# Optimization experiments

Measured on AMD Instinct MI355X. Metric: run time of the kernel, lower is better.

Reference implementation:

```python
import jax, jax.numpy as jnp
import numpy as np

# Config (matches init_kwargs): range [-32,32]^3, voxel 0.5 -> 128^3 grid; BEV 200x200
PC_LOW = np.array([-32.0, -32.0, -32.0], dtype=np.float32)
PC_HIGH = np.array([32.0, 32.0, 32.0], dtype=np.float32)
VOX = 0.5
G = 128
BEV_H, BEV_W = 200, 200
BN_EPS = 1e-5
STRIDES = [1, 2, 1, 2, 1, 1]


def setup_inputs() -> dict:
    key = jax.random.key(0)
    ks = jax.random.split(key, 10)
    N = 2_000_000
    xyz = jax.random.uniform(ks[0], (N, 3), jnp.float32, minval=-32.0, maxval=32.0)
    inten = jax.random.uniform(ks[1], (N, 1), jnp.float32)
    points = jnp.concatenate([xyz, inten], axis=1)  # (N,4)
    chans = [(32, 4), (64, 32), (64, 64), (128, 64), (128, 128), (256, 128)]
    inp = {"points": points}
    for i, (co, ci) in enumerate(chans):
        fan_in = ci * 27
        inp[f"w{i+1}"] = jax.random.normal(ks[2 + i], (co, ci, 3, 3, 3), jnp.float32) / np.sqrt(fan_in)
        inp[f"g{i+1}"] = jnp.ones((co,), jnp.float32)
        inp[f"b{i+1}"] = jnp.zeros((co,), jnp.float32)
    return inp


def _voxelize(points):
    # range filtering + floor-binning + clamp, faithful to voxelize_points (dense path: scatter-ADD)
    low = jnp.asarray(PC_LOW)
    high = jnp.asarray(PC_HIGH)
    mask = jnp.all((points[:, :3] >= low) & (points[:, :3] <= high), axis=1)
    coords = jnp.floor((points[:, :3] - low) / VOX).astype(jnp.int32)
    coords = jnp.clip(coords, 0, G - 1)
    vals = points * mask[:, None].astype(points.dtype)  # invalid points contribute 0
    # original indexes voxel_grid[:, z, y, x]
    grid = jnp.zeros((G, G, G, 4), points.dtype)
    grid = grid.at[coords[:, 2], coords[:, 1], coords[:, 0]].add(vals)
    return jnp.transpose(grid, (3, 0, 1, 2))  # (4, G, G, G)


def _conv3d(x, w, s):
    # PyTorch Conv3d(k=3, padding=1, stride=s), NCDHW
    return jax.lax.conv_general_dilated(
        x, w, window_strides=(s, s, s), padding=[(1, 1), (1, 1), (1, 1)],
        dimension_numbers=("NCDHW", "OIDHW", "NCDHW"))


def _bn_relu(x, g, b):
    # eval-mode BN: running_mean=0, running_var=1
    scale = (g / jnp.sqrt(1.0 + BN_EPS))[None, :, None, None, None]
    return jax.nn.relu(x * scale + b[None, :, None, None, None])


def reference(points, w1, w2, w3, w4, w5, w6,
              g1, g2, g3, g4, g5, g6,
              b1, b2, b3, b4, b5, b6):
    ws = [w1, w2, w3, w4, w5, w6]
    gs = [g1, g2, g3, g4, g5, g6]
    bs = [b1, b2, b3, b4, b5, b6]
    x = _voxelize(points)[None]  # (1,4,G,G,G)
    for w, g, b, s in zip(ws, gs, bs, STRIDES):
        x = _bn_relu(_conv3d(x, w, s), g, b)
    feat = x[0]  # (256, G/4, G/4, G/4)
    bev = jnp.max(feat, axis=2)  # torch.max(..., dim=2) on (C,D1,D2,D3) -> (C,D1,D3)
    # F.interpolate bilinear align_corners=False == jax.image.resize half-pixel bilinear
    bev = jax.image.resize(bev, (bev.shape[0], BEV_H, BEV_W), method="bilinear")
    return bev
```

## Files before the change

### kernel.cpp

```cpp
#include <hip/hip_runtime.h>
#include <hip/hip_fp16.h>
#include <cstdint>
#include <cstddef>

typedef __attribute__((ext_vector_type(8))) short short8;
typedef __attribute__((ext_vector_type(8))) _Float16 half8;
typedef __attribute__((ext_vector_type(16))) float f32x16;

__device__ __forceinline__ float bf2f(unsigned short u) { return __uint_as_float(((unsigned)u) << 16); }
__device__ __forceinline__ unsigned short f2bf(float f) {
    unsigned u = __float_as_uint(f);
    return (unsigned short)((u + 0x7fffu + ((u >> 16) & 1u)) >> 16);
}
__device__ __forceinline__ void sync_lds() {
    asm volatile("s_waitcnt lgkmcnt(0)\n\ts_barrier" ::: "memory");
}

static constexpr float BN_INV = 0.9999950000374997f;


__device__ __forceinline__ int vox_bucket(float4 p, bool& ok) {
    ok = !(p.x < -32.f || p.x > 32.f || p.y < -32.f || p.y > 32.f || p.z < -32.f || p.z > 32.f);
    int cy = min(max((int)floorf((p.y + 32.f) * 2.f), 0), 127);
    int cz = min(max((int)floorf((p.z + 32.f) * 2.f), 0), 127);
    return cz * 4 + (cy >> 5);
}

__global__ __launch_bounds__(256) void vox_count(const float4* __restrict__ pts,
                                                 int* __restrict__ cnt, int N) {
    __shared__ int h[512];
    for (int t = threadIdx.x; t < 512; t += 256) h[t] = 0;
    __syncthreads();
    int stride = gridDim.x * 256;
    for (int i = blockIdx.x * 256 + threadIdx.x; i < N; i += stride) {
        float4 p = pts[i];
        bool ok;
        int bk = vox_bucket(p, ok);
        if (ok) atomicAdd(&h[bk], 1);
    }
    __syncthreads();
    for (int t = threadIdx.x; t < 512; t += 256)
        if (h[t]) atomicAdd(&cnt[t], h[t]);
}

__global__ void vox_scan(const int* __restrict__ cnt, int* __restrict__ off,
                         int* __restrict__ cur) {
    __shared__ int c[512];
    int t = threadIdx.x;
    c[t] = cnt[t];
    __syncthreads();
    int s = 0;
    for (int i = 0; i < t; ++i) s += c[i];
    off[t] = s;
    cur[t] = s;
}

__global__ __launch_bounds__(256) void vox_scatter(const float4* __restrict__ pts,
                                                   int* __restrict__ cur,
                                                   float4* __restrict__ sorted, int N) {
    __shared__ int h[512];
    __shared__ int base[512];
    int b0 = blockIdx.x * 4096;
    for (int t = threadIdx.x; t < 512; t += 256) h[t] = 0;
    __syncthreads();
    float4 p[16];
    int bk[16];
#pragma unroll
    for (int j = 0; j < 16; ++j) {
        int i = b0 + j * 256 + threadIdx.x;
        bk[j] = -1;
        if (i < N) {
            p[j] = pts[i];
            bool ok;
            int b = vox_bucket(p[j], ok);
            if (ok) {
                bk[j] = b;
                atomicAdd(&h[b], 1);
            }
        }
    }
    __syncthreads();
    for (int t = threadIdx.x; t < 512; t += 256) {
        int n = h[t];
        base[t] = n ? atomicAdd(&cur[t], n) : 0;
        h[t] = 0;
    }
    __syncthreads();
#pragma unroll
    for (int j = 0; j < 16; ++j) {
        if (bk[j] >= 0) {
            int r = atomicAdd(&h[bk[j]], 1);
            sorted[base[bk[j]] + r] = p[j];
        }
    }
}

__global__ __launch_bounds__(256) void vox_accum(const float4* __restrict__ sorted,
                                                 const int* __restrict__ off,
                                                 const int* __restrict__ cnt,
                                                 __half2* __restrict__ grid) {
    __shared__ float s[32 * 128 * 4];
    for (int t = threadIdx.x; t < 16384; t += 256) s[t] = 0.f;
    __syncthreads();
    int bid = blockIdx.x;
    int bz = bid >> 2;
    int ylo = (bid & 3) << 5;
    int b = off[bid], n = cnt[bid];
    for (int i = threadIdx.x; i < n; i += 256) {
        float4 p = sorted[b + i];
        int cx = min(max((int)floorf((p.x + 32.f) * 2.f), 0), 127);
        int cy = min(max((int)floorf((p.y + 32.f) * 2.f), 0), 127);
        float* v = s + ((cy - ylo) * 128 + cx) * 4;
        unsafeAtomicAdd(v + 0, p.x);
        unsafeAtomicAdd(v + 1, p.y);
        unsafeAtomicAdd(v + 2, p.z);
        unsafeAtomicAdd(v + 3, p.w);
    }
    __syncthreads();
    for (int t = threadIdx.x; t < 4096; t += 256) {
        int ry = t >> 7, cx = t & 127;
        const float* v = s + t * 4;
        union { __half2 h[2]; float2 f; } u;
        u.h[0] = __floats2half2_rn(v[0], v[1]);
        u.h[1] = __floats2half2_rn(v[2], v[3]);
        int gi = (((bz + 1) * 130 + (ylo + ry + 1)) * 130 + (cx + 1)) * 2;
        *(float2*)(grid + gi) = u.f;
    }
}

__global__ __launch_bounds__(256) void pad_zero(unsigned short* __restrict__ buf,
                                                int Xp, int Zp, int C) {
    const int cpc = (C >= 8) ? (C / 8) : 1;
    long i = (long)blockIdx.x * 256 + threadIdx.x;
    long nz = (long)2 * Xp * Xp;
    long ny = (long)(Zp - 2) * 2 * Xp;
    long nx = (long)(Zp - 2) * (Xp - 2) * 2;
    long total = (nz + ny + nx) * cpc;
    if (i >= total) return;
    long cell = i / cpc;
    int ch = (int)(i - cell * cpc) * 8;
    int z, y, x;
    if (cell < nz) {
        long r = cell;
        z = (r >= (long)Xp * Xp) ? (Zp - 1) : 0;
        r %= (long)Xp * Xp;
        y = (int)(r / Xp);
        x = (int)(r % Xp);
    } else if (cell < nz + ny) {
        long r = cell - nz;
        z = 1 + (int)(r / (2 * Xp));
        int s = (int)(r % (2 * Xp));
        y = (s >= Xp) ? (Xp - 1) : 0;
        x = (s >= Xp) ? (s - Xp) : s;
    } else {
        long r = cell - nz - ny;
        z = 1 + (int)(r / ((Xp - 2) * 2));
        int s = (int)(r % ((Xp - 2) * 2));
        y = 1 + (s >> 1);
        x = (s & 1) ? (Xp - 1) : 0;
    }
    unsigned short* p = buf + (((long)z * Xp + y) * Xp + x) * C + ch;
    if (C >= 8) {
        *(short8*)p = (short8){0, 0, 0, 0, 0, 0, 0, 0};
    } else {
        *(float2*)p = (float2){0.f, 0.f};
    }
}
static inline int pad_blocks(int Xp, int Zp, int C) {
    long cells = (long)2 * Xp * Xp + (long)(Zp - 2) * 2 * Xp + (long)(Zp - 2) * (Xp - 2) * 2;
    long thr = cells * ((C >= 8) ? (C / 8) : 1);
    return (int)((thr + 255) / 256);
}

__global__ __launch_bounds__(256) void repack_w(const float* __restrict__ w, const float* __restrict__ g,
                                                unsigned short* __restrict__ o, int Co, int CI) {
    int i = blockIdx.x * 256 + threadIdx.x;
    int total = 27 * Co * CI;
    if (i >= total) return;
    int ci = i % CI;
    int t = i / CI;
    int co = t % Co;
    int k = t / Co;
    float v = w[((size_t)(co * CI + ci)) * 27 + k] * g[co] * BN_INV;
    o[i] = f2bf(v);
}
__global__ __launch_bounds__(256) void repack_w1m(const float* __restrict__ w, const float* __restrict__ g,
                                                  unsigned short* __restrict__ o) {
    int i = blockIdx.x * 256 + threadIdx.x;
    if (i >= 9 * 32 * 16) return;
    int k16 = i & 15;
    int co = (i >> 4) & 31;
    int p = i >> 9;
    float v = 0.f;
    if (k16 < 12) {
        int dx = k16 >> 2, ci = k16 & 3;
        int dz = p / 3, dy = p % 3;
        v = w[(co * 4 + ci) * 27 + dz * 9 + dy * 3 + dx] * g[co] * BN_INV;
    }
    o[i] = __half_as_ushort(__float2half(v));
}

__global__ __launch_bounds__(256) void conv1_mfma(
    const unsigned short* __restrict__ in, const unsigned short* __restrict__ wa,
    const float* __restrict__ beta, unsigned short* __restrict__ out,
    int zstart, int r0) {
    const int tid = threadIdx.x;
    const int l31 = tid & 31;
    const int lh = (tid >> 5) & 1;
    const int wv = tid >> 6;
    int v = blockIdx.x * 128 + wv * 32 + l31;
    int x = v & 127;
    int y = (v >> 7) & 127;
    int z = zstart + (v >> 14);

    const unsigned short* base = in + ((z * 130 + y) * 130 + x) * 4 + lh * 8;
    uint2 d0[9], d1[9];
    half8 a[9];
#pragma unroll
    for (int p = 0; p < 9; ++p) {
        int dz = p / 3, dy = p % 3;
        const unsigned short* rp = base + (dz * 130 + dy) * 520;
        d0[p] = *(const uint2*)(rp);
        d1[p] = *(const uint2*)(rp + 4);
        a[p] = *(const half8*)(wa + (p * 32 + l31) * 16 + lh * 8);
    }
    f32x16 acc = {0.f};
#pragma unroll
    for (int p = 0; p < 9; ++p) {
        uint4 braw = {d0[p].x, d0[p].y, d1[p].x, d1[p].y};
        half8 b = *(half8*)&braw;
        acc = __builtin_amdgcn_mfma_f32_32x32x16_f16(a[p], b, acc, 0, 0, 0);
    }
    int r = z - zstart + r0;
    int ob = ((r * 130 + (y + 1)) * 130 + (x + 1)) * 32;
#pragma unroll
    for (int g = 0; g < 4; ++g) {
        int cb = 4 * lh + 8 * g;
        float4 bt = *(const float4*)(beta + cb);
        ushort4 u;
        u.x = f2bf(fmaxf(acc[g * 4 + 0] + bt.x, 0.f));
        u.y = f2bf(fmaxf(acc[g * 4 + 1] + bt.y, 0.f));
        u.z = f2bf(fmaxf(acc[g * 4 + 2] + bt.z, 0.f));
        u.w = f2bf(fmaxf(acc[g * 4 + 3] + bt.w, 0.f));
        *(ushort4*)(out + ob + cb) = u;
    }
}

template <int CI, int KC, int S>
__global__ __launch_bounds__(256) void conv_mfma(
    const unsigned short* __restrict__ in, const unsigned short* __restrict__ wb,
    const float* __restrict__ beta, unsigned short* __restrict__ out,
    int D, int lgD, int Xp, int Xpo, int Co, int zin_base, int v_off) {

    constexpr int KCp = KC + 8;
    constexpr int OPB = KC / 8;
    constexpr int NB = KC / 16;
    constexpr int NA = KC / 32;
    constexpr int NCH = KC / 16;
    constexpr int NCC = CI / KC;
    constexpr int STOT = 27 * NCC;

    __shared__ __align__(16) short sA[2 * 64 * KCp];
    __shared__ __align__(16) short sB[2 * 128 * KCp];

    const int tid = threadIdx.x;
    const int l31 = tid & 31;
    const int lh = (tid >> 5) & 1;
    const int wv = tid >> 6;

    const unsigned gx = gridDim.x;
    const unsigned lin = blockIdx.y * gx + blockIdx.x;
    const unsigned q = (gx * gridDim.y) >> 3;
    const unsigned lin2 = (lin & 7) * q + (lin >> 3);
    const unsigned bxs = lin2 % gx;
    const unsigned bys = lin2 / gx;
    const int co0 = bxs * 64;

    int bgIdx[NB], blB[NB];
#pragma unroll
    for (int j = 0; j < NB; ++j) {
        int idx = tid + j * 256;
        int vL = idx / OPB;
        int oct = idx - vL * OPB;
        int vg = v_off + bys * 128 + vL;
        int x = vg & (D - 1);
        int ry = vg >> lgD;
        int y = ry & (D - 1);
        int z = ry >> lgD;
        bgIdx[j] = ((z * S * Xp + y * S) * Xp + x * S) * CI + oct * 8;
        blB[j] = vL * KCp + oct * 8;
    }
    int agIdx[NA], alA[NA];
#pragma unroll
    for (int j = 0; j < NA; ++j) {
        int idx = tid + j * 256;
        int cA = idx / OPB;
        int oct = idx - cA * OPB;
        agIdx[j] = (co0 + cA) * CI + oct * 8;
        alA[j] = cA * KCp + oct * 8;
    }
    const int bfr = (wv * 32 + l31) * KCp + lh * 8;
    const int afr = l31 * KCp + lh * 8;

    short8 rB[2][NB], rA[2][NA];

    auto loadStage = [&](int s, int r) {
        int k = s / NCC;
        int c0 = (s - k * NCC) * KC;
        int dz = k / 9;
        int rr = k - dz * 9;
        int dy = rr / 3;
        int dx = rr - dy * 3;
        int kb = (((dz - zin_base) * Xp + dy) * Xp + dx) * CI + c0;
        int ka = k * Co * CI + c0;
#pragma unroll
        for (int j = 0; j < NB; ++j) rB[r][j] = *(const short8*)(in + bgIdx[j] + kb);
#pragma unroll
        for (int j = 0; j < NA; ++j) rA[r][j] = *(const short8*)(wb + agIdx[j] + ka);
    };
    auto storeLDS = [&](int r, int buf) {
#pragma unroll
        for (int j = 0; j < NB; ++j) *(short8*)(sB + buf * 128 * KCp + blB[j]) = rB[r][j];
#pragma unroll
        for (int j = 0; j < NA; ++j) *(short8*)(sA + buf * 64 * KCp + alA[j]) = rA[r][j];
    };

    f32x16 acc0 = {0.f}, acc1 = {0.f};

    loadStage(0, 0);
    loadStage(1, 1);
    storeLDS(0, 0);
    sync_lds();

#pragma unroll
    for (int s = 0; s < STOT; ++s) {
        if (s + 2 < STOT) loadStage(s + 2, s & 1);
        const short* pB = sB + (s & 1) * 128 * KCp + bfr;
        const short* pA = sA + (s & 1) * 64 * KCp + afr;
#pragma unroll
        for (int c = 0; c < NCH; ++c) {
            short8 bv = *(const short8*)(pB + c * 16);
            short8 a0 = *(const short8*)(pA + c * 16);
            short8 a1 = *(const short8*)(pA + 32 * KCp + c * 16);
            acc0 = __builtin_amdgcn_mfma_f32_32x32x16_bf16(a0, bv, acc0, 0, 0, 0);
            acc1 = __builtin_amdgcn_mfma_f32_32x32x16_bf16(a1, bv, acc1, 0, 0, 0);
        }
        if (s + 1 < STOT) {
            storeLDS((s + 1) & 1, (s + 1) & 1);
            sync_lds();
        }
    }

    int vg = v_off + bys * 128 + wv * 32 + l31;
    int x = vg & (D - 1);
    int ry = vg >> lgD;
    int y = ry & (D - 1);
    int z = ry >> lgD;
    size_t ob = (((size_t)(z + 1) * Xpo + (y + 1)) * Xpo + (x + 1)) * Co + co0;
#pragma unroll
    for (int cot = 0; cot < 2; ++cot) {
        const f32x16& a = cot ? acc1 : acc0;
#pragma unroll
        for (int g = 0; g < 4; ++g) {
            int cb = cot * 32 + 4 * lh + 8 * g;
            float4 bt = *(const float4*)(beta + co0 + cb);
            ushort4 u;
            u.x = f2bf(fmaxf(a[g * 4 + 0] + bt.x, 0.f));
            u.y = f2bf(fmaxf(a[g * 4 + 1] + bt.y, 0.f));
            u.z = f2bf(fmaxf(a[g * 4 + 2] + bt.z, 0.f));
            u.w = f2bf(fmaxf(a[g * 4 + 3] + bt.w, 0.f));
            *(ushort4*)(out + ob + cb) = u;
        }
    }
}

__global__ __launch_bounds__(256) void bev_max_kernel(const unsigned short* __restrict__ feat,
                                                      float* __restrict__ bev) {
    int z = blockIdx.x >> 5;
    int x = blockIdx.x & 31;
    int c = threadIdx.x;
    const unsigned short* p = feat + ((((z + 1) * 34) + 1) * 34 + (x + 1)) * 256 + c;
    float mx = 0.f;
#pragma unroll
    for (int y = 0; y < 32; ++y) mx = fmaxf(mx, bf2f(p[y * 34 * 256]));
    bev[(z * 32 + x) * 256 + c] = mx;
}

__global__ __launch_bounds__(256) void resize_kernel(const float* __restrict__ bev,
                                                     float* __restrict__ out) {
    int i = blockIdx.x * 256 + threadIdx.x;
    if (i >= 256 * 200 * 200) return;
    int ox = i % 200;
    int t = i / 200;
    int oy = t % 200;
    int c = t / 200;
    const float sc = 32.0f / 200.0f;
    float fy = (oy + 0.5f) * sc - 0.5f;
    float fx = (ox + 0.5f) * sc - 0.5f;
    float fy0 = floorf(fy), fx0 = floorf(fx);
    float ty = fy - fy0, tx = fx - fx0;
    int y0 = min(max((int)fy0, 0), 31), y1 = min(max((int)fy0 + 1, 0), 31);
    int x0 = min(max((int)fx0, 0), 31), x1 = min(max((int)fx0 + 1, 0), 31);
    float v00 = bev[(y0 * 32 + x0) * 256 + c], v01 = bev[(y0 * 32 + x1) * 256 + c];
    float v10 = bev[(y1 * 32 + x0) * 256 + c], v11 = bev[(y1 * 32 + x1) * 256 + c];
    float top = v00 + tx * (v01 - v00);
    float bot = v10 + tx * (v11 - v10);
    out[i] = top + ty * (bot - top);
}

extern "C" void kernel_launch(void* const* d_in, const int* in_sizes, int n_in,
                              void* d_out, int out_size, void* d_ws, size_t ws_size,
                              hipStream_t stream) {
    const float* points = (const float*)d_in[0];
    int N = in_sizes[0] / 4;
    const float *W[6], *G[6], *B[6];
    for (int i = 0; i < 6; ++i) {
        W[i] = (const float*)d_in[1 + 3 * i];
        G[i] = (const float*)d_in[2 + 3 * i];
        B[i] = (const float*)d_in[3 + 3 * i];
    }

    char* ws = (char*)d_ws;
    const size_t MiB = 1ull << 20;
    unsigned short* gridH = (unsigned short*)(ws);
    int* cnt = (int*)(ws + 17580032);
    int* off = cnt + 512;
    int* cur = off + 512;
    float4* sorted = (float4*)(ws + 18 * MiB);
    unsigned short* O1s = (unsigned short*)(ws + 18 * MiB);
    unsigned short* O2p = (unsigned short*)(ws + 104 * MiB);
    unsigned short* O3p = (unsigned short*)(ws);
    unsigned short* O4p = (unsigned short*)(ws + 37 * MiB);
    unsigned short* O5p = (unsigned short*)(ws + 48 * MiB);
    unsigned short* O6p = (unsigned short*)(ws + 59 * MiB);
    float* bev = (float*)(ws + 80 * MiB);
    unsigned short* wc1 = (unsigned short*)(ws + 140 * MiB);
    unsigned short* wb2 = (unsigned short*)(ws + 140 * MiB + 16384);
    unsigned short* wb3 = wb2 + 27 * 64 * 32;
    unsigned short* wb4 = wb3 + 27 * 64 * 64;
    unsigned short* wb5 = wb4 + 27 * 128 * 64;
    unsigned short* wb6 = wb5 + 27 * 128 * 128;

    repack_w1m<<<18, 256, 0, stream>>>(W[0], G[0], wc1);
    repack_w<<<216, 256, 0, stream>>>(W[1], G[1], wb2, 64, 32);
    repack_w<<<432, 256, 0, stream>>>(W[2], G[2], wb3, 64, 64);
    repack_w<<<864, 256, 0, stream>>>(W[3], G[3], wb4, 128, 64);
    repack_w<<<1728, 256, 0, stream>>>(W[4], G[4], wb5, 128, 128);
    repack_w<<<3456, 256, 0, stream>>>(W[5], G[5], wb6, 256, 128);

    pad_zero<<<pad_blocks(130, 130, 4), 256, 0, stream>>>(gridH, 130, 130, 4);
    hipMemsetAsync(cnt, 0, 2048, stream);
    pad_zero<<<pad_blocks(66, 66, 64), 256, 0, stream>>>(O2p, 66, 66, 64);
    vox_count<<<1024, 256, 0, stream>>>((const float4*)points, cnt, N);
    vox_scan<<<1, 512, 0, stream>>>(cnt, off, cur);
    vox_scatter<<<(N + 4095) / 4096, 256, 0, stream>>>((const float4*)points, cur, sorted, N);
    vox_accum<<<512, 256, 0, stream>>>(sorted, off, cnt, (__half2*)gridH);

    pad_zero<<<pad_blocks(130, 65, 32), 256, 0, stream>>>(O1s, 130, 65, 32);
    conv1_mfma<<<8192, 256, 0, stream>>>(gridH, wc1, B[0], O1s, 0, 1);
    conv_mfma<32, 32, 2><<<dim3(1, 1024), 256, 0, stream>>>(O1s, wb2, B[1], O2p, 64, 6, 130, 66, 64, 0, 0);
    conv1_mfma<<<8320, 256, 0, stream>>>(gridH, wc1, B[0], O1s, 63, 0);
    conv_mfma<32, 32, 2><<<dim3(1, 1024), 256, 0, stream>>>(O1s, wb2, B[1], O2p, 64, 6, 130, 66, 64, 64, 131072);

    pad_zero<<<pad_blocks(66, 66, 64), 256, 0, stream>>>(O3p, 66, 66, 64);
    pad_zero<<<pad_blocks(34, 34, 128), 256, 0, stream>>>(O4p, 34, 34, 128);
    pad_zero<<<pad_blocks(34, 34, 128), 256, 0, stream>>>(O5p, 34, 34, 128);
    pad_zero<<<pad_blocks(34, 34, 256), 256, 0, stream>>>(O6p, 34, 34, 256);

    conv_mfma<64, 64, 1><<<dim3(1, 2048), 256, 0, stream>>>(O2p, wb3, B[2], O3p, 64, 6, 66, 66, 64, 0, 0);
    conv_mfma<64, 64, 2><<<dim3(2, 256), 256, 0, stream>>>(O3p, wb4, B[3], O4p, 32, 5, 66, 34, 128, 0, 0);
    conv_mfma<128, 64, 1><<<dim3(2, 256), 256, 0, stream>>>(O4p, wb5, B[4], O5p, 32, 5, 34, 34, 128, 0, 0);
    conv_mfma<128, 64, 1><<<dim3(4, 256), 256, 0, stream>>>(O5p, wb6, B[5], O6p, 32, 5, 34, 34, 256, 0, 0);

    bev_max_kernel<<<1024, 256, 0, stream>>>(O6p, bev);
    resize_kernel<<<40000, 256, 0, stream>>>(bev, (float*)d_out);
}
```

Baseline: 645.3 us.

## Use direct global-to-LDS loads with double-buffered pipeline for conv layers 3-6

```diff
diff --git a/kernel.cpp b/kernel.cpp
--- a/kernel.cpp
+++ b/kernel.cpp
@@ -14,6 +14,14 @@
 }
 __device__ __forceinline__ void sync_lds() {
     asm volatile("s_waitcnt lgkmcnt(0)\n\ts_barrier" ::: "memory");
+}
+__device__ __forceinline__ void sync_vm() {
+    asm volatile("s_waitcnt vmcnt(0)\n\ts_barrier" ::: "memory");
+}
+__device__ __forceinline__ void gload16(const unsigned short* g, char* l) {
+    __builtin_amdgcn_global_load_lds(
+        (const __attribute__((address_space(1))) unsigned int*)g,
+        (__attribute__((address_space(3))) unsigned int*)l, 16, 0, 0);
 }
 
 static constexpr float BN_INV = 0.9999950000374997f;
@@ -374,6 +382,119 @@
     }
 }
 
+template <int CI, int S>
+__global__ __launch_bounds__(256, 3) void conv_mfma_g(
+    const unsigned short* __restrict__ in, const unsigned short* __restrict__ wb,
+    const float* __restrict__ beta, unsigned short* __restrict__ out,
+    int D, int lgD, int Xp, int Xpo, int Co, int zin_base, int v_off) {
+
+    constexpr int KC = 64;
+    constexpr int NCC = CI / KC;
+    constexpr int STOT = 27 * NCC;
+
+    __shared__ __align__(16) char sB[2 * 128 * 128];
+    __shared__ __align__(16) char sA[2 * 64 * 128];
+
+    const int tid = threadIdx.x;
+    const int l31 = tid & 31;
+    const int lh = (tid >> 5) & 1;
+    const int wv = tid >> 6;
+    const int l63 = tid & 63;
+
+    const unsigned gx = gridDim.x;
+    const unsigned lin = blockIdx.y * gx + blockIdx.x;
+    const unsigned q = (gx * gridDim.y) >> 3;
+    const unsigned lin2 = (lin & 7) * q + (lin >> 3);
+    const unsigned bxs = lin2 % gx;
+    const unsigned bys = lin2 / gx;
+    const int co0 = bxs * 64;
+
+    const int swoct = (l63 & 7) ^ (l63 >> 3);
+
+    int bgIdxG[4];
+#pragma unroll
+    for (int j = 0; j < 4; ++j) {
+        int r = (j * 4 + wv) * 8 + (l63 >> 3);
+        int vg = v_off + bys * 128 + r;
+        int x = vg & (D - 1);
+        int ry = vg >> lgD;
+        int y = ry & (D - 1);
+        int z = ry >> lgD;
+        bgIdxG[j] = ((z * S * Xp + y * S) * Xp + x * S) * CI + swoct * 8;
+    }
+    int agIdxG[2];
+#pragma unroll
+    for (int j = 0; j < 2; ++j) {
+        int r = (j * 4 + wv) * 8 + (l63 >> 3);
+        agIdxG[j] = (co0 + r) * CI + swoct * 8;
+    }
+
+    auto issueStage = [&](int s, int buf) {
+        int k = s / NCC;
+        int c0 = (s - k * NCC) * KC;
+        int dz = k / 9;
+        int rr = k - dz * 9;
+        int dy = rr / 3;
+        int dx = rr - dy * 3;
+        int kb = (((dz - zin_base) * Xp + dy) * Xp + dx) * CI + c0;
+        int ka = k * Co * CI + c0;
+#pragma unroll
+        for (int j = 0; j < 4; ++j)
+            gload16(in + bgIdxG[j] + kb, sB + buf * 16384 + (j * 4 + wv) * 1024);
+#pragma unroll
+        for (int j = 0; j < 2; ++j)
+            gload16(wb + agIdxG[j] + ka, sA + buf * 8192 + (j * 4 + wv) * 1024);
+    };
+
+    const int brow = wv * 32 + l31;
+    const int r7 = l31 & 7;
+
+    f32x16 acc0 = {0.f}, acc1 = {0.f};
+
+    issueStage(0, 0);
+    sync_vm();
+
+#pragma unroll
+    for (int s = 0; s < STOT; ++s) {
+        if (s + 1 < STOT) issueStage(s + 1, (s + 1) & 1);
+        const char* pB = sB + (s & 1) * 16384 + brow * 128;
+        const char* pA0 = sA + (s & 1) * 8192 + l31 * 128;
+        const char* pA1 = pA0 + 32 * 128;
+#pragma unroll
+        for (int c = 0; c < 4; ++c) {
+            int oct = ((2 * c + lh) ^ r7) * 16;
+            short8 bv = *(const short8*)(pB + oct);
+            short8 a0 = *(const short8*)(pA0 + oct);
+            short8 a1 = *(const short8*)(pA1 + oct);
+            acc0 = __builtin_amdgcn_mfma_f32_32x32x16_bf16(a0, bv, acc0, 0, 0, 0);
+            acc1 = __builtin_amdgcn_mfma_f32_32x32x16_bf16(a1, bv, acc1, 0, 0, 0);
+        }
+        sync_vm();
+    }
+
+    int vg = v_off + bys * 128 + wv * 32 + l31;
+    int x = vg & (D - 1);
+    int ry = vg >> lgD;
+    int y = ry & (D - 1);
+    int z = ry >> lgD;
+    size_t ob = (((size_t)(z + 1) * Xpo + (y + 1)) * Xpo + (x + 1)) * Co + co0;
+#pragma unroll
+    for (int cot = 0; cot < 2; ++cot) {
+        const f32x16& a = cot ? acc1 : acc0;
+#pragma unroll
+        for (int g = 0; g < 4; ++g) {
+            int cb = cot * 32 + 4 * lh + 8 * g;
+            float4 bt = *(const float4*)(beta + co0 + cb);
+            ushort4 u;
+            u.x = f2bf(fmaxf(a[g * 4 + 0] + bt.x, 0.f));
+            u.y = f2bf(fmaxf(a[g * 4 + 1] + bt.y, 0.f));
+            u.z = f2bf(fmaxf(a[g * 4 + 2] + bt.z, 0.f));
+            u.w = f2bf(fmaxf(a[g * 4 + 3] + bt.w, 0.f));
+            *(ushort4*)(out + ob + cb) = u;
+        }
+    }
+}
+
 __global__ __launch_bounds__(256) void bev_max_kernel(const unsigned short* __restrict__ feat,
                                                       float* __restrict__ bev) {
     int z = blockIdx.x >> 5;
@@ -467,10 +588,10 @@
     pad_zero<<<pad_blocks(34, 34, 128), 256, 0, stream>>>(O5p, 34, 34, 128);
     pad_zero<<<pad_blocks(34, 34, 256), 256, 0, stream>>>(O6p, 34, 34, 256);
 
-    conv_mfma<64, 64, 1><<<dim3(1, 2048), 256, 0, stream>>>(O2p, wb3, B[2], O3p, 64, 6, 66, 66, 64, 0, 0);
-    conv_mfma<64, 64, 2><<<dim3(2, 256), 256, 0, stream>>>(O3p, wb4, B[3], O4p, 32, 5, 66, 34, 128, 0, 0);
-    conv_mfma<128, 64, 1><<<dim3(2, 256), 256, 0, stream>>>(O4p, wb5, B[4], O5p, 32, 5, 34, 34, 128, 0, 0);
-    conv_mfma<128, 64, 1><<<dim3(4, 256), 256, 0, stream>>>(O5p, wb6, B[5], O6p, 32, 5, 34, 34, 256, 0, 0);
+    conv_mfma_g<64, 1><<<dim3(1, 2048), 256, 0, stream>>>(O2p, wb3, B[2], O3p, 64, 6, 66, 66, 64, 0, 0);
+    conv_mfma_g<64, 2><<<dim3(2, 256), 256, 0, stream>>>(O3p, wb4, B[3], O4p, 32, 5, 66, 34, 128, 0, 0);
+    conv_mfma_g<128, 1><<<dim3(2, 256), 256, 0, stream>>>(O4p, wb5, B[4], O5p, 32, 5, 34, 34, 128, 0, 0);
+    conv_mfma_g<128, 1><<<dim3(4, 256), 256, 0, stream>>>(O5p, wb6, B[5], O6p, 32, 5, 34, 34, 256, 0, 0);
 
     bev_max_kernel<<<1024, 256, 0, stream>>>(O6p, bev);
     resize_kernel<<<40000, 256, 0, stream>>>(bev, (float*)d_out);
```

Result: slower. 677.3 us (+5.0%).
